# Kernel tuning notes

Hardware: AMD Instinct MI355X
Metric: run time of the kernel (lower is better)

Reference implementation:

```python
import jax, jax.numpy as jnp
import numpy as np

H = 128; W = 128; WH = 8; WW = 8; SH = 4; SW = 4
DIM = 512; HEADS = 16; HD = DIM // HEADS; HIDDEN = 2048
NH = H // WH; NW = W // WW; NWIN = NH * NW; WL = WH * WW
EPS = 1e-5
SCALE = HD ** -0.5


def _rel_pos_index():
    # Swin-style relative position index, static (WL, WL) int table
    coords = np.stack(np.meshgrid(np.arange(WH), np.arange(WW), indexing='ij')).reshape(2, -1)
    rel = (coords[:, :, None] - coords[:, None, :]).transpose(1, 2, 0)  # (WL, WL, 2)
    rel[:, :, 0] += WH - 1
    rel[:, :, 1] += WW - 1
    rel[:, :, 0] *= 2 * WW - 1
    return rel.sum(-1)  # (WL, WL), values in [0, (2WH-1)(2WW-1))


def _shift_attn_mask():
    # static shifted-window attention mask, (NWIN, WL, WL)
    m = np.zeros((H, W))
    cnt = 0
    for hs in (slice(0, -WH), slice(-WH, -SH), slice(-SH, None)):
        for ws in (slice(0, -WW), slice(-WW, -SW), slice(-SW, None)):
            m[hs, ws] = cnt
            cnt += 1
    mw = m.reshape(NH, WH, NW, WW).transpose(0, 2, 1, 3).reshape(NWIN, WL)
    am = mw[:, None, :] - mw[:, :, None]
    return np.where(am != 0, -100.0, 0.0).astype(np.float32)


_RPI = _rel_pos_index()
_MASK = _shift_attn_mask()


def _layernorm(x, w, b):
    mu = x.mean(-1, keepdims=True)
    var = ((x - mu) ** 2).mean(-1, keepdims=True)
    return (x - mu) / jnp.sqrt(var + EPS) * w + b


def _win_part(x):  # (H, W, D) -> (NWIN, WL, D)
    return x.reshape(NH, WH, NW, WW, DIM).transpose(0, 2, 1, 3, 4).reshape(NWIN, WL, DIM)


def _win_rev(w):  # (NWIN, WL, D) -> (H, W, D)
    return w.reshape(NH, NW, WH, WW, DIM).transpose(0, 2, 1, 3, 4).reshape(H, W, DIM)


def setup_inputs() -> dict:
    key = jax.random.key(0)
    ks = jax.random.split(key, 8)
    s = 0.02
    return {
        'x': jax.random.normal(ks[0], (H * W, DIM), dtype=jnp.float32),
        'ln1_w': jnp.ones((DIM,), jnp.float32),
        'ln1_b': jnp.zeros((DIM,), jnp.float32),
        'ln2_w': jnp.ones((DIM,), jnp.float32),
        'ln2_b': jnp.zeros((DIM,), jnp.float32),
        'qkv_w': jax.random.normal(ks[1], (3 * DIM, DIM), dtype=jnp.float32) * s,
        'qkv_b': jnp.zeros((3 * DIM,), jnp.float32),
        'proj_w': jax.random.normal(ks[2], (DIM, DIM), dtype=jnp.float32) * s,
        'proj_b': jnp.zeros((DIM,), jnp.float32),
        'rpb': jax.random.normal(ks[3], ((2 * WH - 1) * (2 * WW - 1), HEADS), dtype=jnp.float32) * s,
        'mlp_w1': jax.random.normal(ks[4], (HIDDEN, DIM), dtype=jnp.float32) * s,
        'mlp_b1': jnp.zeros((HIDDEN,), jnp.float32),
        'mlp_w2': jax.random.normal(ks[5], (DIM, HIDDEN), dtype=jnp.float32) * s,
        'mlp_b2': jnp.zeros((DIM,), jnp.float32),
    }


def reference(x, ln1_w, ln1_b, ln2_w, ln2_b, qkv_w, qkv_b, proj_w, proj_b, rpb,
              mlp_w1, mlp_b1, mlp_w2, mlp_b2):
    skip = x
    h = _layernorm(x, ln1_w, ln1_b).reshape(H, W, DIM)
    # cyclic shift + window partition
    h = jnp.roll(h, shift=(-SH, -SW), axis=(0, 1))
    xw = _win_part(h)  # (NWIN, WL, DIM)
    # windowed multi-head self-attention (equinox Linear: y = W @ x + b)
    qkv = jnp.einsum('nld,ed->nle', xw, qkv_w) + qkv_b
    q, k, v = [t.reshape(NWIN, WL, HEADS, HD).transpose(0, 2, 1, 3)
               for t in jnp.split(qkv, 3, axis=-1)]  # each (NWIN, HEADS, WL, HD)
    attn = jnp.einsum('nhqd,nhkd->nhqk', q * SCALE, k)
    bias = rpb[_RPI.reshape(-1)].reshape(WL, WL, HEADS).transpose(2, 0, 1)  # (HEADS, WL, WL)
    attn = attn + bias[None] + jnp.asarray(_MASK)[:, None]
    attn = jax.nn.softmax(attn, axis=-1)
    out = jnp.einsum('nhqk,nhkd->nhqd', attn, v).transpose(0, 2, 1, 3).reshape(NWIN, WL, DIM)
    out = jnp.einsum('nld,ed->nle', out, proj_w) + proj_b
    # window reverse + reverse cyclic shift
    h = jnp.roll(_win_rev(out), shift=(SH, SW), axis=(0, 1)).reshape(H * W, DIM)
    h = skip + h  # residual (drop_path is Identity at rate 0)
    # FFN branch (note: original code does x = x + drop_path(x), i.e. 2*mlp(norm2(.)))
    h = _layernorm(h, ln2_w, ln2_b)
    m = jax.nn.gelu(jnp.einsum('ld,ed->le', h, mlp_w1) + mlp_b1)
    m = jnp.einsum('le,de->ld', m, mlp_w2) + mlp_b2
    return m + m
```

## Files before the change

### kernel.cpp

```cpp
#include <hip/hip_runtime.h>
#include <hip/hip_bf16.h>
#include <stdint.h>

#define TOK   16384
#define DIMM  512
#define NHEAD 16
#define HDIM  32
#define HID   2048
#define NWIN  256
#define WLEN  64
#define EPSV  1e-5f
#define SCL   0.17677669529663687f

typedef __hip_bfloat16 bf16;
typedef __attribute__((ext_vector_type(8))) __bf16 bf16x8;
typedef __attribute__((ext_vector_type(4))) float f32x4;

__device__ __forceinline__ int remap_row(int r){
  int win = r >> 6, l = r & 63;
  int gh = ((win >> 4) << 3) + (l >> 3);
  int gw = ((win & 15) << 3) + (l & 7);
  int oh = (gh + 4) & 127, ow = (gw + 4) & 127;
  return (oh << 7) + ow;
}

__device__ __forceinline__ int region_of(int win, int l){
  int gh = ((win >> 4) << 3) + (l >> 3);
  int gw = ((win & 15) << 3) + (l & 7);
  int rh = (gh < 120) ? 0 : ((gh < 124) ? 1 : 2);
  int rw = (gw < 120) ? 0 : ((gw < 124) ? 1 : 2);
  return rh * 3 + rw;
}

__device__ __forceinline__ void gl_lds16(const bf16* g, bf16* l){
  __builtin_amdgcn_global_load_lds((const __attribute__((address_space(1))) void*)g,
                                   (__attribute__((address_space(3))) void*)l, 16, 0, 0);
}

__global__ __launch_bounds__(256) void convert_w(const float* __restrict__ a,
                                                 const float* __restrict__ b,
                                                 const float* __restrict__ c,
                                                 const float* __restrict__ d,
                                                 bf16* __restrict__ dst){
  int e = (blockIdx.x * 256 + threadIdx.x) * 4;
  float4 v;
  if (e < 786432)        v = *(const float4*)(a + e);
  else if (e < 1048576)  v = *(const float4*)(b + (e - 786432));
  else if (e < 2097152)  v = *(const float4*)(c + (e - 1048576));
  else                   v = *(const float4*)(d + (e - 2097152));
  union { bf16 h[4]; int2 q; } u;
  u.h[0] = __float2bfloat16(v.x); u.h[1] = __float2bfloat16(v.y);
  u.h[2] = __float2bfloat16(v.z); u.h[3] = __float2bfloat16(v.w);
  *(int2*)(dst + e) = u.q;
}

template<bool REMAP>
__global__ __launch_bounds__(256) void ln_kernel(const float* __restrict__ in,
    const float* __restrict__ w, const float* __restrict__ b, bf16* __restrict__ outp)
{
  const int wave = threadIdx.x >> 6, lane = threadIdx.x & 63;
  const int r = blockIdx.x * 4 + wave;
  const int src = REMAP ? remap_row(r) : r;
  const float4* row = (const float4*)(in + (size_t)src * DIMM);
  float4 v0 = row[lane*2], v1 = row[lane*2 + 1];
  float sm = v0.x+v0.y+v0.z+v0.w + v1.x+v1.y+v1.z+v1.w;
  float sq = v0.x*v0.x+v0.y*v0.y+v0.z*v0.z+v0.w*v0.w
           + v1.x*v1.x+v1.y*v1.y+v1.z*v1.z+v1.w*v1.w;
  #pragma unroll
  for (int off = 1; off < 64; off <<= 1){
    sm += __shfl_xor(sm, off);
    sq += __shfl_xor(sq, off);
  }
  const float mean = sm * (1.f/512.f);
  const float rstd = rsqrtf(sq*(1.f/512.f) - mean*mean + EPSV);
  const float4* wp = (const float4*)w; const float4* bp = (const float4*)b;
  float4 w0 = wp[lane*2], w1 = wp[lane*2+1], b0 = bp[lane*2], b1 = bp[lane*2+1];
  union { bf16 h[8]; int4 q; } u;
  u.h[0] = __float2bfloat16((v0.x-mean)*rstd*w0.x + b0.x);
  u.h[1] = __float2bfloat16((v0.y-mean)*rstd*w0.y + b0.y);
  u.h[2] = __float2bfloat16((v0.z-mean)*rstd*w0.z + b0.z);
  u.h[3] = __float2bfloat16((v0.w-mean)*rstd*w0.w + b0.w);
  u.h[4] = __float2bfloat16((v1.x-mean)*rstd*w1.x + b1.x);
  u.h[5] = __float2bfloat16((v1.y-mean)*rstd*w1.y + b1.y);
  u.h[6] = __float2bfloat16((v1.z-mean)*rstd*w1.z + b1.z);
  u.h[7] = __float2bfloat16((v1.w-mean)*rstd*w1.w + b1.w);
  *(int4*)(outp + (size_t)r*DIMM + lane*8) = u.q;
}

#define M_QKV  0
#define M_PROJ 1
#define M_MLP1 2
#define M_MLP2 3

template<int MODE, int K>
__global__ __launch_bounds__(256) void gemm_bt(const bf16* __restrict__ A,
    const bf16* __restrict__ Wt, const float* __restrict__ bias,
    bf16* __restrict__ out_b, float* __restrict__ out_f, const float* __restrict__ skip)
{
  __shared__ bf16 lsA[128*32];
  __shared__ bf16 lsB[128*32];
  const int tid = threadIdx.x, wave = tid >> 6, lane = tid & 63;
  const int lrow = lane & 15, lgrp = lane >> 4;
  const int m0 = blockIdx.x * 128, n0 = blockIdx.y * 128;
  const int wr = (wave >> 1) * 64, wc = (wave & 1) * 64;

  f32x4 acc[4][4] = {};

  const bf16* Abase = A  + (size_t)m0 * K;
  const bf16* Bbase = Wt + (size_t)n0 * K;
  const int srow = tid >> 2;
  const int scol = (tid & 3) * 8;

  #define STAGE(kt) { \
    gl_lds16(Abase + (size_t)(srow)      * K + (kt) + scol, lsA + wave*512); \
    gl_lds16(Abase + (size_t)(srow + 64) * K + (kt) + scol, lsA + 2048 + wave*512); \
    gl_lds16(Bbase + (size_t)(srow)      * K + (kt) + scol, lsB + wave*512); \
    gl_lds16(Bbase + (size_t)(srow + 64) * K + (kt) + scol, lsB + 2048 + wave*512); \
  }

  STAGE(0);
  __syncthreads();
  for (int kt = 0; kt < K; kt += 32){
    bf16x8 af[4], bfv[4];
    #pragma unroll
    for (int i = 0; i < 4; i++){
      af[i]  = *(const bf16x8*)(lsA + (wr + i*16 + lrow)*32 + lgrp*8);
      bfv[i] = *(const bf16x8*)(lsB + (wc + i*16 + lrow)*32 + lgrp*8);
    }
    #pragma unroll
    for (int i = 0; i < 4; i++)
      #pragma unroll
      for (int j = 0; j < 4; j++)
        acc[i][j] = __builtin_amdgcn_mfma_f32_16x16x32_bf16(af[i], bfv[j], acc[i][j], 0, 0, 0);
    __syncthreads();
    if (kt + 32 < K){
      STAGE(kt + 32);
      __syncthreads();
    }
  }
  #undef STAGE

  #pragma unroll
  for (int i = 0; i < 4; i++){
    #pragma unroll
    for (int j = 0; j < 4; j++){
      const int col   = n0 + wc + j*16 + lrow;
      const int row_b = m0 + wr + i*16 + lgrp*4;
      const float bv = bias[col];
      #pragma unroll
      for (int rr = 0; rr < 4; rr++){
        const int row = row_b + rr;
        float v = acc[i][j][rr] + bv;
        if constexpr (MODE == M_QKV){
          const int t = col >> 9, rem = col & 511;
          const int head = rem >> 5, hd = rem & 31;
          const int win = row >> 6, l = row & 63;
          out_b[(size_t)t * (TOK*DIMM) + ((size_t)(win*NHEAD + head)*WLEN + l)*HDIM + hd]
              = __float2bfloat16(v);
        } else if constexpr (MODE == M_PROJ){
          const int o = remap_row(row);
          out_f[(size_t)o*DIMM + col] = v + skip[(size_t)o*DIMM + col];
        } else if constexpr (MODE == M_MLP1){
          const float x3 = v*v*v;
          const float g = 0.5f*v*(1.f + tanhf(0.7978845608028654f*(v + 0.044715f*x3)));
          out_b[(size_t)row*HID + col] = __float2bfloat16(g);
        } else {
          out_f[(size_t)row*DIMM + col] = 2.f * v;
        }
      }
    }
  }
}

__global__ __launch_bounds__(256) void attn_kernel(const bf16* __restrict__ qkv,
    const float* __restrict__ rpb, bf16* __restrict__ outp)
{
  __shared__ bf16 Pl[4][64][72];
  const int wave = threadIdx.x >> 6, lane = threadIdx.x & 63;
  const int lrow = lane & 15, lgrp = lane >> 4;
  const int wh = blockIdx.x * 4 + wave;
  const int win = wh >> 4, head = wh & 15;
  const bf16* qb = qkv + (size_t)wh * (WLEN*HDIM);
  const bf16* kb = qb + (size_t)TOK * DIMM;
  const bf16* vb = kb + (size_t)TOK * DIMM;

  bf16x8 aq[4], ak[4];
  #pragma unroll
  for (int i = 0; i < 4; i++){
    aq[i] = *(const bf16x8*)(qb + (i*16 + lrow)*HDIM + lgrp*8);
    ak[i] = *(const bf16x8*)(kb + (i*16 + lrow)*HDIM + lgrp*8);
  }
  f32x4 s[4][4] = {};
  #pragma unroll
  for (int i = 0; i < 4; i++)
    #pragma unroll
    for (int j = 0; j < 4; j++)
      s[i][j] = __builtin_amdgcn_mfma_f32_16x16x32_bf16(aq[i], ak[j], s[i][j], 0, 0, 0);

  #pragma unroll
  for (int i = 0; i < 4; i++){
    #pragma unroll
    for (int rr = 0; rr < 4; rr++){
      const int srow = i*16 + lgrp*4 + rr;
      const int rq = region_of(win, srow);
      float vals[4]; float mx = -1e30f;
      #pragma unroll
      for (int j = 0; j < 4; j++){
        const int scol = j*16 + lrow;
        const int idx = ((srow>>3) - (scol>>3) + 7)*15 + ((srow&7) - (scol&7) + 7);
        float v = s[i][j][rr]*SCL + rpb[idx*NHEAD + head];
        if (region_of(win, scol) != rq) v -= 100.f;
        vals[j] = v; mx = fmaxf(mx, v);
      }
      mx = fmaxf(mx, __shfl_xor(mx, 1));
      mx = fmaxf(mx, __shfl_xor(mx, 2));
      mx = fmaxf(mx, __shfl_xor(mx, 4));
      mx = fmaxf(mx, __shfl_xor(mx, 8));
      float sum = 0.f;
      #pragma unroll
      for (int j = 0; j < 4; j++){ vals[j] = __expf(vals[j] - mx); sum += vals[j]; }
      sum += __shfl_xor(sum, 1); sum += __shfl_xor(sum, 2);
      sum += __shfl_xor(sum, 4); sum += __shfl_xor(sum, 8);
      const float rs = 1.f / sum;
      #pragma unroll
      for (int j = 0; j < 4; j++)
        Pl[wave][srow][j*16 + lrow] = __float2bfloat16(vals[j] * rs);
    }
  }

  f32x4 o[4][2] = {};
  const __bf16* vraw = (const __bf16*)vb;
  #pragma unroll
  for (int st = 0; st < 2; st++){
    bf16x8 pa[4];
    #pragma unroll
    for (int i = 0; i < 4; i++)
      pa[i] = *(const bf16x8*)(&Pl[wave][i*16 + lrow][st*32 + lgrp*8]);
    bf16x8 bv[2];
    #pragma unroll
    for (int j = 0; j < 2; j++){
      #pragma unroll
      for (int jj = 0; jj < 8; jj++)
        bv[j][jj] = vraw[(size_t)(st*32 + lgrp*8 + jj)*HDIM + j*16 + lrow];
    }
    #pragma unroll
    for (int i = 0; i < 4; i++)
      #pragma unroll
      for (int j = 0; j < 2; j++)
        o[i][j] = __builtin_amdgcn_mfma_f32_16x16x32_bf16(pa[i], bv[j], o[i][j], 0, 0, 0);
  }
  bf16* orow = outp + (size_t)win * WLEN * DIMM + head * HDIM;
  #pragma unroll
  for (int i = 0; i < 4; i++)
    #pragma unroll
    for (int j = 0; j < 2; j++)
      #pragma unroll
      for (int rr = 0; rr < 4; rr++){
        const int l = i*16 + lgrp*4 + rr;
        orow[(size_t)l * DIMM + j*16 + lrow] = __float2bfloat16(o[i][j][rr]);
      }
}

extern "C" void kernel_launch(void* const* d_in, const int* in_sizes, int n_in,
                              void* d_out, int out_size, void* d_ws, size_t ws_size,
                              hipStream_t stream) {
  const float* x     = (const float*)d_in[0];
  const float* ln1w  = (const float*)d_in[1];
  const float* ln1b  = (const float*)d_in[2];
  const float* ln2w  = (const float*)d_in[3];
  const float* ln2b  = (const float*)d_in[4];
  const float* qkvw  = (const float*)d_in[5];
  const float* qkvbi = (const float*)d_in[6];
  const float* projw = (const float*)d_in[7];
  const float* projb = (const float*)d_in[8];
  const float* rpb   = (const float*)d_in[9];
  const float* m1w   = (const float*)d_in[10];
  const float* m1b   = (const float*)d_in[11];
  const float* m2w   = (const float*)d_in[12];
  const float* m2b   = (const float*)d_in[13];

  bf16* wqkv  = (bf16*)d_ws;
  bf16* wproj = wqkv + 786432;
  bf16* wm1   = wproj + 262144;
  bf16* wm2   = wm1 + 1048576;
  bf16* xw    = wm2 + 1048576;
  float* hbuf = (float*)(xw + 8388608);
  bf16* qkvb  = (bf16*)(hbuf + 8388608);
  bf16* attno = qkvb + 3*(size_t)8388608;
  bf16* m1buf = qkvb;
  bf16* h2    = xw;

  convert_w<<<3072, 256, 0, stream>>>(qkvw, projw, m1w, m2w, wqkv);
  ln_kernel<true><<<4096, 256, 0, stream>>>(x, ln1w, ln1b, xw);
  { dim3 g(TOK/128, 1536/128);
    gemm_bt<M_QKV, 512><<<g, 256, 0, stream>>>(xw, wqkv, qkvbi, qkvb, nullptr, nullptr); }
  attn_kernel<<<1024, 256, 0, stream>>>(qkvb, rpb, attno);
  { dim3 g(TOK/128, 512/128);
    gemm_bt<M_PROJ, 512><<<g, 256, 0, stream>>>(attno, wproj, projb, nullptr, hbuf, x); }
  ln_kernel<false><<<4096, 256, 0, stream>>>(hbuf, ln2w, ln2b, h2);
  { dim3 g(TOK/128, 2048/128);
    gemm_bt<M_MLP1, 512><<<g, 256, 0, stream>>>(h2, wm1, m1b, m1buf, nullptr, nullptr); }
  { dim3 g(TOK/128, 512/128);
    gemm_bt<M_MLP2, 2048><<<g, 256, 0, stream>>>(m1buf, wm2, m2b, nullptr, (float*)d_out, nullptr); }
}
```

Measured before the change: 230.6 us.

## Double-buffer GEMM LDS tiles and use sigmoid-form GELU in MLP1 epilogue

```diff
diff --git a/kernel.cpp b/kernel.cpp
--- a/kernel.cpp
+++ b/kernel.cpp
@@ -97,8 +97,8 @@
     const bf16* __restrict__ Wt, const float* __restrict__ bias,
     bf16* __restrict__ out_b, float* __restrict__ out_f, const float* __restrict__ skip)
 {
-  __shared__ bf16 lsA[128*32];
-  __shared__ bf16 lsB[128*32];
+  __shared__ bf16 lsA[2][128*32];
+  __shared__ bf16 lsB[2][128*32];
   const int tid = threadIdx.x, wave = tid >> 6, lane = tid & 63;
   const int lrow = lane & 15, lgrp = lane >> 4;
   const int m0 = blockIdx.x * 128, n0 = blockIdx.y * 128;
@@ -111,21 +111,23 @@
   const int srow = tid >> 2;
   const int scol = (tid & 3) * 8;
 
-  #define STAGE(kt) { \
-    gl_lds16(Abase + (size_t)(srow)      * K + (kt) + scol, lsA + wave*512); \
-    gl_lds16(Abase + (size_t)(srow + 64) * K + (kt) + scol, lsA + 2048 + wave*512); \
-    gl_lds16(Bbase + (size_t)(srow)      * K + (kt) + scol, lsB + wave*512); \
-    gl_lds16(Bbase + (size_t)(srow + 64) * K + (kt) + scol, lsB + 2048 + wave*512); \
-  }
-
-  STAGE(0);
+  #define STAGE(kt, bf) { \
+    gl_lds16(Abase + (size_t)(srow)      * K + (kt) + scol, lsA[bf] + wave*512); \
+    gl_lds16(Abase + (size_t)(srow + 64) * K + (kt) + scol, lsA[bf] + 2048 + wave*512); \
+    gl_lds16(Bbase + (size_t)(srow)      * K + (kt) + scol, lsB[bf] + wave*512); \
+    gl_lds16(Bbase + (size_t)(srow + 64) * K + (kt) + scol, lsB[bf] + 2048 + wave*512); \
+  }
+
+  STAGE(0, 0);
   __syncthreads();
+  int cur = 0;
   for (int kt = 0; kt < K; kt += 32){
+    if (kt + 32 < K) STAGE(kt + 32, cur ^ 1);
     bf16x8 af[4], bfv[4];
     #pragma unroll
     for (int i = 0; i < 4; i++){
-      af[i]  = *(const bf16x8*)(lsA + (wr + i*16 + lrow)*32 + lgrp*8);
-      bfv[i] = *(const bf16x8*)(lsB + (wc + i*16 + lrow)*32 + lgrp*8);
+      af[i]  = *(const bf16x8*)(lsA[cur] + (wr + i*16 + lrow)*32 + lgrp*8);
+      bfv[i] = *(const bf16x8*)(lsB[cur] + (wc + i*16 + lrow)*32 + lgrp*8);
     }
     #pragma unroll
     for (int i = 0; i < 4; i++)
@@ -133,10 +135,7 @@
       for (int j = 0; j < 4; j++)
         acc[i][j] = __builtin_amdgcn_mfma_f32_16x16x32_bf16(af[i], bfv[j], acc[i][j], 0, 0, 0);
     __syncthreads();
-    if (kt + 32 < K){
-      STAGE(kt + 32);
-      __syncthreads();
-    }
+    cur ^= 1;
   }
   #undef STAGE
 
@@ -161,8 +160,8 @@
           const int o = remap_row(row);
           out_f[(size_t)o*DIMM + col] = v + skip[(size_t)o*DIMM + col];
         } else if constexpr (MODE == M_MLP1){
-          const float x3 = v*v*v;
-          const float g = 0.5f*v*(1.f + tanhf(0.7978845608028654f*(v + 0.044715f*x3)));
+          const float u = 1.5957691216057308f * (v + 0.044715f*v*v*v);
+          const float g = v * (1.0f / (1.0f + __expf(-u)));
           out_b[(size_t)row*HID + col] = __float2bfloat16(g);
         } else {
           out_f[(size_t)row*DIMM + col] = 2.f * v;
```

Result: no change. 227.6 us (-1.3%).
